# Optimization experiments

Hardware: AMD Instinct MI355X
Metric: run time of the kernel (lower is better)

## Reference

```python
import jax, jax.numpy as jnp
import numpy as np

N_NODES = 100000
N_EDGES = 1600000


def _glorot(key, shape):
    fan_in, fan_out = shape[0], shape[1]
    lim = np.sqrt(6.0 / (fan_in + fan_out))
    return jax.random.uniform(key, shape, jnp.float32, -lim, lim)


def setup_inputs() -> dict:
    key = jax.random.key(0)
    ks = jax.random.split(key, 8)
    x = jax.random.normal(ks[0], (N_NODES, 2), jnp.float32)
    edge_index = jax.random.randint(ks[1], (2, N_EDGES), 0, N_NODES, jnp.int32)
    return {
        "x": x,
        "edge_index": edge_index,
        "W1": _glorot(ks[2], (2, 64)),
        "b1": jnp.zeros((64,), jnp.float32),
        "W2": _glorot(ks[3], (64, 64)),
        "b2": jnp.zeros((64,), jnp.float32),
        "W3": _glorot(ks[4], (64, 64)),
        "b3": jnp.zeros((64,), jnp.float32),
        "fw1": _glorot(ks[5], (64, 128)),
        "fb1": jnp.zeros((128,), jnp.float32),
        "fw2": _glorot(ks[6], (128, 32)),
        "fb2": jnp.zeros((32,), jnp.float32),
    }


def _gcn_norm(edge_index, n_nodes, dtype):
    # PyG GCNConv default: add self-loops, symmetric normalization.
    loop = jnp.arange(n_nodes, dtype=edge_index.dtype)
    src = jnp.concatenate([edge_index[0], loop])
    dst = jnp.concatenate([edge_index[1], loop])
    deg = jax.ops.segment_sum(jnp.ones_like(dst, dtype), dst, num_segments=n_nodes)
    dinv = jnp.where(deg > 0, jax.lax.rsqrt(jnp.maximum(deg, 1e-12)), 0.0)
    norm = dinv[src] * dinv[dst]  # [E + N]
    return src, dst, norm


def _gcn_layer(h, src, dst, norm, n_nodes, W, b):
    h = h @ W                                   # [N, C_out] transform first (C_out small)
    msg = h[src] * norm[:, None]                # gather + per-edge scale
    out = jax.ops.segment_sum(msg, dst, num_segments=n_nodes)  # scatter-add
    return out + b


def reference(x, edge_index, W1, b1, W2, b2, W3, b3, fw1, fb1, fw2, fb2):
    n = x.shape[0]
    src, dst, norm = _gcn_norm(edge_index, n, x.dtype)
    h = jax.nn.relu(_gcn_layer(x, src, dst, norm, n, W1, b1))
    h = jax.nn.relu(_gcn_layer(h, src, dst, norm, n, W2, b2))
    h = jax.nn.relu(_gcn_layer(h, src, dst, norm, n, W3, b3))
    h = jax.nn.relu(h @ fw1 + fb1)  # fc1
    return h @ fw2 + fb2            # fc2 -> bottleneck latent
```

## Files before the change

kernel.cpp:

```cpp
#include <hip/hip_runtime.h>
#include <hip/hip_bf16.h>

#define NN 100000
#define NE 1600000
#define NBUK 1563
#define NBB  196
#define BATCH 8192
#define CNTSZ (NBUK*NBB)
#define SCANB 300

using bf16 = __hip_bfloat16;
typedef unsigned short us8_t __attribute__((ext_vector_type(8)));
static __device__ __forceinline__ float b2f(bf16 v){ return __bfloat162float(v); }
static __device__ __forceinline__ bf16 f2b(float v){ return __float2bfloat16(v); }
static __device__ __forceinline__ float us2f(unsigned u){
  unsigned x = u<<16; float f; __builtin_memcpy(&f,&x,4); return f;
}
static __device__ __forceinline__ unsigned short f2us(float v){
  bf16 b = f2b(v); unsigned short u; __builtin_memcpy(&u,&b,2); return u;
}

#define W1F   0
#define B1F   128
#define W2F   192
#define B2F   4288
#define W3F   4352
#define B3F   8448
#define FW1F  8512
#define FB1F  16704
#define FW2F  16832
#define FB2F  20928
#define WTOT  20960

__global__ void k_flag0(int* flag){ if(threadIdx.x==0) *flag = 0; }
__global__ void k_sniffB(const unsigned short* __restrict__ xr, int* flag){
  __shared__ int found;
  if(threadIdx.x==0) found = 0;
  __syncthreads();
  int loc = 0;
  for(int si = blockIdx.x*256 + threadIdx.x; si < 100000; si += 98*256){
    unsigned e = (xr[si*2]>>7)&0xFF;
    if(e==0xFFu || e==0u) loc = 1;
  }
  if(loc) found = 1;
  __syncthreads();
  if(threadIdx.x==0 && found) atomicOr(flag, 1);
}

__global__ void k_convert_w(const void* p0,const void* p1,const void* p2,const void* p3,
                            const void* p4,const void* p5,const void* p6,const void* p7,
                            const void* p8,const void* p9,
                            const int* __restrict__ flag, float* __restrict__ Wc){
  int t = blockIdx.x*256 + threadIdx.x;
  if(t >= WTOT) return;
  const void* ps[10] = {p0,p1,p2,p3,p4,p5,p6,p7,p8,p9};
  const int off[11] = {W1F,B1F,W2F,B2F,W3F,B3F,FW1F,FB1F,FW2F,FB2F,WTOT};
  int seg = 0;
  while(off[seg+1] <= t) seg++;
  int j = t - off[seg];
  Wc[t] = (*flag) ? ((const float*)ps[seg])[j] : b2f(((const bf16*)ps[seg])[j]);
}

__global__ void k_bhist(const int* __restrict__ dst, int* __restrict__ cnt){
  __shared__ int hist[NBUK];
  for(int j=threadIdx.x; j<NBUK; j+=512) hist[j] = 0;
  __syncthreads();
  int e0 = blockIdx.x*BATCH;
  int e1 = min(NE, e0+BATCH);
  int q0 = e0>>2, q1 = e1>>2;
  const int4* d4 = (const int4*)dst;
  for(int q=q0+threadIdx.x; q<q1; q+=512){
    int4 d = d4[q];
    atomicAdd(&hist[d.x>>6], 1);
    atomicAdd(&hist[d.y>>6], 1);
    atomicAdd(&hist[d.z>>6], 1);
    atomicAdd(&hist[d.w>>6], 1);
  }
  __syncthreads();
  for(int j=threadIdx.x; j<NBUK; j+=512) cnt[j*NBB + blockIdx.x] = hist[j];
}
__global__ void k_scanA(const int* __restrict__ cnt, int* __restrict__ tmp,
                        int* __restrict__ bsum){
  __shared__ int sh[1024];
  int gi = blockIdx.x*1024 + threadIdx.x;
  int v = (gi < CNTSZ) ? cnt[gi] : 0;
  sh[threadIdx.x] = v; __syncthreads();
  for(int off=1; off<1024; off<<=1){
    int t = (threadIdx.x>=off) ? sh[threadIdx.x-off] : 0;
    __syncthreads();
    sh[threadIdx.x] += t;
    __syncthreads();
  }
  if(gi < CNTSZ) tmp[gi] = sh[threadIdx.x];
  if(threadIdx.x == 1023) bsum[blockIdx.x] = sh[1023];
}
__global__ void k_scanB(const int* __restrict__ bsum, int* __restrict__ boff){
  __shared__ int sh[512];
  int v = (threadIdx.x < SCANB) ? bsum[threadIdx.x] : 0;
  sh[threadIdx.x] = v; __syncthreads();
  for(int off=1; off<512; off<<=1){
    int t = (threadIdx.x>=off) ? sh[threadIdx.x-off] : 0;
    __syncthreads();
    sh[threadIdx.x] += t;
    __syncthreads();
  }
  boff[threadIdx.x] = sh[threadIdx.x] - v;
}
__global__ void k_scanC(int* __restrict__ cnt, const int* __restrict__ tmp,
                        const int* __restrict__ boff, int* __restrict__ bucketStart){
  int gi = blockIdx.x*1024 + threadIdx.x;
  if(gi < CNTSZ){
    int orig = cnt[gi];
    int excl = tmp[gi] - orig + boff[gi>>10];
    cnt[gi] = excl;
    if(gi % NBB == 0) bucketStart[gi/NBB] = excl;
  }
  if(gi == 0) bucketStart[NBUK] = NE;
}
__global__ void k_bplace(const int* __restrict__ src, const int* __restrict__ dst,
                         const int* __restrict__ cnt, int* __restrict__ epk){
  __shared__ int cur[NBUK];
  for(int j=threadIdx.x; j<NBUK; j+=512) cur[j] = cnt[j*NBB + blockIdx.x];
  __syncthreads();
  int e0 = blockIdx.x*BATCH, e1 = min(NE, e0+BATCH);
  int q0 = e0>>2, q1 = e1>>2;
  const int4* d4 = (const int4*)dst;
  const int4* s4 = (const int4*)src;
  for(int q=q0+threadIdx.x; q<q1; q+=512){
    int4 d = d4[q];
    int4 s = s4[q];
    int p0 = atomicAdd(&cur[d.x>>6], 1);
    int p1 = atomicAdd(&cur[d.y>>6], 1);
    int p2 = atomicAdd(&cur[d.z>>6], 1);
    int p3 = atomicAdd(&cur[d.w>>6], 1);
    epk[p0] = (s.x<<6) | (d.x&63);
    epk[p1] = (s.y<<6) | (d.y&63);
    epk[p2] = (s.z<<6) | (d.z&63);
    epk[p3] = (s.w<<6) | (d.w&63);
  }
}
__global__ void k_bsort(const int* __restrict__ bucketStart, const int* __restrict__ epk,
                        int* __restrict__ srcS, int* __restrict__ rowptr,
                        float* __restrict__ dinv, const void* __restrict__ xv,
                        const int* __restrict__ flag, float2* __restrict__ xd){
  __shared__ int hist[64], excl[64], cur[64];
  int tid = threadIdx.x;
  if(tid < 64) hist[tid] = 0;
  __syncthreads();
  int b = blockIdx.x, beg = bucketStart[b], end = bucketStart[b+1];
  for(int p=beg+tid; p<end; p+=512) atomicAdd(&hist[epk[p]&63], 1);
  __syncthreads();
  if(tid == 0){
    int run = 0;
    for(int j=0;j<64;j++){ excl[j] = run; run += hist[j]; }
  }
  __syncthreads();
  if(tid < 64){
    int g = b*64 + tid;
    if(g < NN){
      rowptr[g] = beg + excl[tid];
      float d = rsqrtf((float)(hist[tid] + 1));
      dinv[g]  = d;
      float x0, x1;
      if(*flag){ float2 p = ((const float2*)xv)[g]; x0=p.x; x1=p.y; }
      else     { const bf16* xp=(const bf16*)xv; x0=b2f(xp[2*g]); x1=b2f(xp[2*g+1]); }
      xd[g] = make_float2(x0*d, x1*d);
    }
    cur[tid] = excl[tid];
  }
  if(b == 0 && tid == 0) rowptr[NN] = NE;
  __syncthreads();
  for(int p=beg+tid; p<end; p+=512){
    int pk = epk[p];
    int pos = atomicAdd(&cur[pk&63], 1);
    srcS[beg+pos] = pk>>6;
  }
}

__global__ void k_prop1(const int* __restrict__ rowptr, const int* __restrict__ srcS,
                        const float2* __restrict__ xd, const float* __restrict__ Wc,
                        const float* __restrict__ dinv, bf16* __restrict__ h){
  __shared__ float W1s[128];
  __shared__ float bs[64];
  if(threadIdx.x < 128) W1s[threadIdx.x] = Wc[W1F + threadIdx.x];
  if(threadIdx.x < 64)  bs[threadIdx.x]  = Wc[B1F + threadIdx.x];
  __syncthreads();
  int i = blockIdx.x*256 + threadIdx.x;
  if(i >= NN) return;
  int beg = rowptr[i], end = rowptr[i+1];
  float2 self = xd[i];
  float ax[8] = {self.x,0,0,0,0,0,0,0};
  float ay[8] = {self.y,0,0,0,0,0,0,0};
  int p = beg;
  for(; p+8 <= end; p += 8){
    int sI[8];
    #pragma unroll
    for(int j=0;j<8;j++) sI[j] = srcS[p+j];
    float2 v[8];
    #pragma unroll
    for(int j=0;j<8;j++) v[j] = xd[sI[j]];
    #pragma unroll
    for(int j=0;j<8;j++){ ax[j] += v[j].x; ay[j] += v[j].y; }
  }
  for(; p<end; p++){ float2 v=xd[srcS[p]]; ax[0]+=v.x; ay[0]+=v.y; }
  float y0 = ((ax[0]+ax[1])+(ax[2]+ax[3]))+((ax[4]+ax[5])+(ax[6]+ax[7]));
  float y1 = ((ay[0]+ay[1])+(ay[2]+ay[3]))+((ay[4]+ay[5])+(ay[6]+ay[7]));
  float d = dinv[i];
  unsigned short* hp = (unsigned short*)h + (size_t)i*64;
  #pragma unroll
  for(int g=0; g<8; g++){
    us8_t o;
    #pragma unroll
    for(int j=0;j<8;j++){
      int c = g*8+j;
      o[j] = f2us(fmaxf(d*(y0*W1s[c] + y1*W1s[64+c]) + bs[c], 0.0f));
    }
    *(us8_t*)(hp + g*8) = o;
  }
}

__global__ void __launch_bounds__(256) k_transform64(
    const bf16* __restrict__ h, const float* __restrict__ W,
    const float* __restrict__ dinv, bf16* __restrict__ s){
  __shared__ float Ws[64*64];
  __shared__ float hs[64][68];
  __shared__ float dl[64];
  int tid = threadIdx.x;
  for(int j=tid; j<4096; j+=256) Ws[j] = W[j];
  int row0 = blockIdx.x*64;
  if(tid < 64){ int r = row0+tid; dl[tid] = (r<NN)? dinv[r] : 0.0f; }
  for(int ch = tid; ch < 512; ch += 256){
    int r = ch>>3, c8 = (ch&7)*8;
    int gr = row0 + r;
    float f[8];
    if(gr < NN){
      us8_t v = *(const us8_t*)((const unsigned short*)h + (size_t)gr*64 + c8);
      #pragma unroll
      for(int j=0;j<8;j++) f[j] = us2f(v[j]);
    } else {
      #pragma unroll
      for(int j=0;j<8;j++) f[j] = 0.0f;
    }
    *(float4*)&hs[r][c8]   = make_float4(f[0],f[1],f[2],f[3]);
    *(float4*)&hs[r][c8+4] = make_float4(f[4],f[5],f[6],f[7]);
  }
  __syncthreads();
  int ty = tid>>4, tx = tid&15;
  float acc[4][4] = {{0}};
  #pragma unroll 8
  for(int k=0;k<64;k++){
    float4 b4 = *(const float4*)&Ws[k*64 + tx*4];
    float a0 = hs[ty*4+0][k];
    float a1 = hs[ty*4+1][k];
    float a2 = hs[ty*4+2][k];
    float a3 = hs[ty*4+3][k];
    acc[0][0] = fmaf(a0,b4.x,acc[0][0]); acc[0][1] = fmaf(a0,b4.y,acc[0][1]);
    acc[0][2] = fmaf(a0,b4.z,acc[0][2]); acc[0][3] = fmaf(a0,b4.w,acc[0][3]);
    acc[1][0] = fmaf(a1,b4.x,acc[1][0]); acc[1][1] = fmaf(a1,b4.y,acc[1][1]);
    acc[1][2] = fmaf(a1,b4.z,acc[1][2]); acc[1][3] = fmaf(a1,b4.w,acc[1][3]);
    acc[2][0] = fmaf(a2,b4.x,acc[2][0]); acc[2][1] = fmaf(a2,b4.y,acc[2][1]);
    acc[2][2] = fmaf(a2,b4.z,acc[2][2]); acc[2][3] = fmaf(a2,b4.w,acc[2][3]);
    acc[3][0] = fmaf(a3,b4.x,acc[3][0]); acc[3][1] = fmaf(a3,b4.y,acc[3][1]);
    acc[3][2] = fmaf(a3,b4.z,acc[3][2]); acc[3][3] = fmaf(a3,b4.w,acc[3][3]);
  }
  #pragma unroll
  for(int rr=0; rr<4; rr++){
    int r = row0 + ty*4 + rr;
    if(r < NN){
      float dv = dl[ty*4+rr];
      unsigned lo = f2us(acc[rr][0]*dv) | ((unsigned)f2us(acc[rr][1]*dv) << 16);
      unsigned hi = f2us(acc[rr][2]*dv) | ((unsigned)f2us(acc[rr][3]*dv) << 16);
      uint2 o; o.x = lo; o.y = hi;
      *(uint2*)((unsigned short*)s + (size_t)r*64 + tx*4) = o;
    }
  }
}

__global__ void __launch_bounds__(256) k_aggregate(
    const int* __restrict__ rowptr, const int* __restrict__ srcS,
    const bf16* __restrict__ s, const float* __restrict__ dinv,
    const float* __restrict__ bias, bf16* __restrict__ h){
  int wave = threadIdx.x>>6, lane = threadIdx.x&63;
  int half = lane>>5;
  int lh   = lane&31;
  int slot = lh>>3;
  int oct  = lane&7;
  int i = blockIdx.x*8 + wave*2 + half;
  int beg = rowptr[i], end = rowptr[i+1];
  unsigned deg = (unsigned)(end - beg);
  const unsigned short* sp = (const unsigned short*)s;
  us8_t sv = *(const us8_t*)(sp + (size_t)i*64 + oct*8);
  float a0[8] = {0,0,0,0,0,0,0,0};
  float a1[8] = {0,0,0,0,0,0,0,0};
  int p0 = beg & ~3;
  while(__any(p0 < end)){
    if(p0 < end){
      int q  = p0 + slot*4;
      int qc = min(q, NE-4);
      int4 E = *(const int4*)(srcS + qc);
      us8_t v0 = *(const us8_t*)(sp + (size_t)E.x*64 + oct*8);
      us8_t v1 = *(const us8_t*)(sp + (size_t)E.y*64 + oct*8);
      us8_t v2 = *(const us8_t*)(sp + (size_t)E.z*64 + oct*8);
      us8_t v3 = *(const us8_t*)(sp + (size_t)E.w*64 + oct*8);
      unsigned rel = (unsigned)(q - beg);
      if(rel+0u < deg){
        #pragma unroll
        for(int j=0;j<8;j++) a0[j] += us2f(v0[j]);
      }
      if(rel+1u < deg){
        #pragma unroll
        for(int j=0;j<8;j++) a1[j] += us2f(v1[j]);
      }
      if(rel+2u < deg){
        #pragma unroll
        for(int j=0;j<8;j++) a0[j] += us2f(v2[j]);
      }
      if(rel+3u < deg){
        #pragma unroll
        for(int j=0;j<8;j++) a1[j] += us2f(v3[j]);
      }
    }
    p0 += 16;
  }
  float c[8];
  #pragma unroll
  for(int j=0;j<8;j++){
    float v = a0[j] + a1[j];
    v += __shfl_xor(v, 8, 64);
    v += __shfl_xor(v, 16, 64);
    c[j] = v;
  }
  float dv = dinv[i];
  float4 bA = *(const float4*)(bias + oct*8);
  float4 bB = *(const float4*)(bias + oct*8 + 4);
  float bb[8] = {bA.x,bA.y,bA.z,bA.w,bB.x,bB.y,bB.z,bB.w};
  us8_t o;
  #pragma unroll
  for(int j=0;j<8;j++){
    float v = c[j] + us2f(sv[j]);
    o[j] = f2us(fmaxf(fmaf(dv, v, bb[j]), 0.0f));
  }
  if(slot == 0)
    *(us8_t*)((unsigned short*)h + (size_t)i*64 + oct*8) = o;
}

__global__ void __launch_bounds__(256) k_fc1(const bf16* __restrict__ h,
                                             const float* __restrict__ Wc,
                                             bf16* __restrict__ f){
  __shared__ float W1s[64*128];
  __shared__ float hs[64][68];
  __shared__ float bs[128];
  int tid = threadIdx.x;
  for(int j=tid; j<8192; j+=256) W1s[j] = Wc[FW1F+j];
  if(tid < 128) bs[tid] = Wc[FB1F+tid];
  int row0 = blockIdx.x*64;
  for(int ch = tid; ch < 512; ch += 256){
    int r = ch>>3, c8 = (ch&7)*8, gr = row0 + r;
    float fv[8];
    if(gr < NN){
      us8_t v = *(const us8_t*)((const unsigned short*)h + (size_t)gr*64 + c8);
      #pragma unroll
      for(int j=0;j<8;j++) fv[j] = us2f(v[j]);
    } else {
      #pragma unroll
      for(int j=0;j<8;j++) fv[j] = 0.0f;
    }
    *(float4*)&hs[r][c8]   = make_float4(fv[0],fv[1],fv[2],fv[3]);
    *(float4*)&hs[r][c8+4] = make_float4(fv[4],fv[5],fv[6],fv[7]);
  }
  __syncthreads();
  int ty = tid>>4, tx = tid&15;
  float acc[4][8] = {{0}};
  #pragma unroll 4
  for(int k=0;k<64;k++){
    float4 b0 = *(const float4*)&W1s[k*128 + tx*8];
    float4 b1 = *(const float4*)&W1s[k*128 + tx*8 + 4];
    float a0 = hs[ty*4+0][k], a1 = hs[ty*4+1][k];
    float a2 = hs[ty*4+2][k], a3 = hs[ty*4+3][k];
    acc[0][0]=fmaf(a0,b0.x,acc[0][0]); acc[0][1]=fmaf(a0,b0.y,acc[0][1]);
    acc[0][2]=fmaf(a0,b0.z,acc[0][2]); acc[0][3]=fmaf(a0,b0.w,acc[0][3]);
    acc[0][4]=fmaf(a0,b1.x,acc[0][4]); acc[0][5]=fmaf(a0,b1.y,acc[0][5]);
    acc[0][6]=fmaf(a0,b1.z,acc[0][6]); acc[0][7]=fmaf(a0,b1.w,acc[0][7]);
    acc[1][0]=fmaf(a1,b0.x,acc[1][0]); acc[1][1]=fmaf(a1,b0.y,acc[1][1]);
    acc[1][2]=fmaf(a1,b0.z,acc[1][2]); acc[1][3]=fmaf(a1,b0.w,acc[1][3]);
    acc[1][4]=fmaf(a1,b1.x,acc[1][4]); acc[1][5]=fmaf(a1,b1.y,acc[1][5]);
    acc[1][6]=fmaf(a1,b1.z,acc[1][6]); acc[1][7]=fmaf(a1,b1.w,acc[1][7]);
    acc[2][0]=fmaf(a2,b0.x,acc[2][0]); acc[2][1]=fmaf(a2,b0.y,acc[2][1]);
    acc[2][2]=fmaf(a2,b0.z,acc[2][2]); acc[2][3]=fmaf(a2,b0.w,acc[2][3]);
    acc[2][4]=fmaf(a2,b1.x,acc[2][4]); acc[2][5]=fmaf(a2,b1.y,acc[2][5]);
    acc[2][6]=fmaf(a2,b1.z,acc[2][6]); acc[2][7]=fmaf(a2,b1.w,acc[2][7]);
    acc[3][0]=fmaf(a3,b0.x,acc[3][0]); acc[3][1]=fmaf(a3,b0.y,acc[3][1]);
    acc[3][2]=fmaf(a3,b0.z,acc[3][2]); acc[3][3]=fmaf(a3,b0.w,acc[3][3]);
    acc[3][4]=fmaf(a3,b1.x,acc[3][4]); acc[3][5]=fmaf(a3,b1.y,acc[3][5]);
    acc[3][6]=fmaf(a3,b1.z,acc[3][6]); acc[3][7]=fmaf(a3,b1.w,acc[3][7]);
  }
  #pragma unroll
  for(int r=0;r<4;r++){
    int gr = row0 + ty*4 + r;
    if(gr < NN){
      us8_t o;
      #pragma unroll
      for(int j=0;j<8;j++) o[j] = f2us(fmaxf(acc[r][j] + bs[tx*8+j], 0.0f));
      *(us8_t*)((unsigned short*)f + (size_t)gr*128 + tx*8) = o;
    }
  }
}

__global__ void __launch_bounds__(256) k_fc2(const bf16* __restrict__ f,
                                             const float* __restrict__ Wc,
                                             const int* __restrict__ flag,
                                             void* __restrict__ outv){
  __shared__ float W2s[128*32];
  __shared__ float fs[64][132];
  __shared__ float bs[32];
  int tid = threadIdx.x;
  for(int j=tid; j<4096; j+=256) W2s[j] = Wc[FW2F+j];
  if(tid < 32) bs[tid] = Wc[FB2F+tid];
  int row0 = blockIdx.x*64;
  for(int ch = tid; ch < 1024; ch += 256){
    int r = ch>>4, c8 = (ch&15)*8, gr = row0 + r;
    float fv[8];
    if(gr < NN){
      us8_t v = *(const us8_t*)((const unsigned short*)f + (size_t)gr*128 + c8);
      #pragma unroll
      for(int j=0;j<8;j++) fv[j] = us2f(v[j]);
    } else {
      #pragma unroll
      for(int j=0;j<8;j++) fv[j] = 0.0f;
    }
    *(float4*)&fs[r][c8]   = make_float4(fv[0],fv[1],fv[2],fv[3]);
    *(float4*)&fs[r][c8+4] = make_float4(fv[4],fv[5],fv[6],fv[7]);
  }
  __syncthreads();
  int ty = tid>>3, tx = tid&7;
  float acc[2][4] = {{0}};
  #pragma unroll 8
  for(int k=0;k<128;k++){
    float4 b4 = *(const float4*)&W2s[k*32 + tx*4];
    float a0 = fs[ty*2+0][k], a1 = fs[ty*2+1][k];
    acc[0][0]=fmaf(a0,b4.x,acc[0][0]); acc[0][1]=fmaf(a0,b4.y,acc[0][1]);
    acc[0][2]=fmaf(a0,b4.z,acc[0][2]); acc[0][3]=fmaf(a0,b4.w,acc[0][3]);
    acc[1][0]=fmaf(a1,b4.x,acc[1][0]); acc[1][1]=fmaf(a1,b4.y,acc[1][1]);
    acc[1][2]=fmaf(a1,b4.z,acc[1][2]); acc[1][3]=fmaf(a1,b4.w,acc[1][3]);
  }
  int fl = *flag;
  #pragma unroll
  for(int r=0;r<2;r++){
    int gr = row0 + ty*2 + r;
    if(gr < NN){
      float o0 = acc[r][0]+bs[tx*4+0], o1 = acc[r][1]+bs[tx*4+1];
      float o2 = acc[r][2]+bs[tx*4+2], o3 = acc[r][3]+bs[tx*4+3];
      if(fl){
        *(float4*)((float*)outv + (size_t)gr*32 + tx*4) = make_float4(o0,o1,o2,o3);
      } else {
        unsigned lo = f2us(o0) | ((unsigned)f2us(o1)<<16);
        unsigned hi = f2us(o2) | ((unsigned)f2us(o3)<<16);
        uint2 o; o.x = lo; o.y = hi;
        *(uint2*)((unsigned short*)outv + (size_t)gr*32 + tx*4) = o;
      }
    }
  }
}

extern "C" void kernel_launch(void* const* d_in, const int* in_sizes, int n_in,
                              void* d_out, int out_size, void* d_ws, size_t ws_size,
                              hipStream_t stream){
  const void* x   = d_in[0];
  const int*  ei  = (const int*)d_in[1];
  const int* srcI = ei;
  const int* dstI = ei + NE;

  char*   base   = (char*)d_ws;
  int*    flag   = (int*)   (base + 0);
  float*  Wc     = (float*) (base + 256);
  int*    bstart = (int*)   (base + 84224);
  int*    cnt    = (int*)   (base + 90624);
  int*    tmpS   = (int*)   (base + 1316096);
  int*    bsum   = (int*)   (base + 2541568);
  int*    boff   = (int*)   (base + 2543616);
  float*  dinv   = (float*) (base + 2545664);
  int*    rowptr = (int*)   (base + 2945664);
  int*    epk    = (int*)   (base + 3345792);
  int*    srcS   = (int*)   (base + 9745792);
  float2* xd     = (float2*)(base + 16145792);
  bf16*   s      = (bf16*)  (base + 16945792);
  bf16*   h      = (bf16*)  (base + 29745792);
  bf16*   f      = (bf16*)  (base + 42545792);

  k_flag0    <<<1, 64, 0, stream>>>(flag);
  k_sniffB   <<<98, 256, 0, stream>>>((const unsigned short*)x, flag);
  k_convert_w<<<(WTOT+255)/256, 256, 0, stream>>>(
      d_in[2], d_in[3], d_in[4], d_in[5], d_in[6],
      d_in[7], d_in[8], d_in[9], d_in[10], d_in[11], flag, Wc);

  k_bhist <<<NBB, 512, 0, stream>>>(dstI, cnt);
  k_scanA <<<SCANB, 1024, 0, stream>>>(cnt, tmpS, bsum);
  k_scanB <<<1, 512, 0, stream>>>(bsum, boff);
  k_scanC <<<SCANB, 1024, 0, stream>>>(cnt, tmpS, boff, bstart);
  k_bplace<<<NBB, 512, 0, stream>>>(srcI, dstI, cnt, epk);
  k_bsort <<<NBUK, 512, 0, stream>>>(bstart, epk, srcS, rowptr, dinv, x, flag, xd);

  k_prop1<<<(NN+255)/256, 256, 0, stream>>>(rowptr, srcS, xd, Wc, dinv, h);

  k_transform64<<<(NN+63)/64, 256, 0, stream>>>(h, Wc+W2F, dinv, s);
  k_aggregate  <<<NN/8, 256, 0, stream>>>(rowptr, srcS, s, dinv, Wc+B2F, h);

  k_transform64<<<(NN+63)/64, 256, 0, stream>>>(h, Wc+W3F, dinv, s);
  k_aggregate  <<<NN/8, 256, 0, stream>>>(rowptr, srcS, s, dinv, Wc+B3F, h);

  k_fc1<<<(NN+63)/64, 256, 0, stream>>>(h, Wc, f);
  k_fc2<<<(NN+63)/64, 256, 0, stream>>>(f, Wc, flag, d_out);
}
```

Baseline: 311.3 us.

## Replace per-block bucket histograms with global atomics and a single-block scan

The bucketing step for the edge sort no longer builds per-block shared histograms with a multi-kernel scan over 1563x196 counts. It now counts edges per bucket with global atomics, scans the 1563 totals in one block, and places edges using global atomic cursors. The flag-reset and sniff kernels are merged into one single-block kernel that also zeroes the counts, and the dinv and bias loads in the aggregate kernel are hoisted ahead of the edge loop. This removes several launches and about 2.4 MB of count traffic, but adds heavy global atomic contention on about 1.5k counters. Edge order inside a bucket also becomes nondeterministic, which can change floating-point summation order.

```diff
diff --git a/kernel.cpp b/kernel.cpp
--- a/kernel.cpp
+++ b/kernel.cpp
@@ -6,8 +6,6 @@
 #define NBUK 1563
 #define NBB  196
 #define BATCH 8192
-#define CNTSZ (NBUK*NBB)
-#define SCANB 300
 
 using bf16 = __hip_bfloat16;
 typedef unsigned short us8_t __attribute__((ext_vector_type(8)));
@@ -32,19 +30,21 @@
 #define FB2F  20928
 #define WTOT  20960
 
-__global__ void k_flag0(int* flag){ if(threadIdx.x==0) *flag = 0; }
-__global__ void k_sniffB(const unsigned short* __restrict__ xr, int* flag){
+__global__ void k_fsniff(const unsigned short* __restrict__ xr, int* __restrict__ flag,
+                         int* __restrict__ cnt){
   __shared__ int found;
-  if(threadIdx.x==0) found = 0;
+  int t = threadIdx.x;
+  if(t==0) found = 0;
+  for(int j=t; j<NBUK; j+=1024) cnt[j] = 0;
   __syncthreads();
   int loc = 0;
-  for(int si = blockIdx.x*256 + threadIdx.x; si < 100000; si += 98*256){
+  for(int si=t; si<NN; si+=1024){
     unsigned e = (xr[si*2]>>7)&0xFF;
     if(e==0xFFu || e==0u) loc = 1;
   }
   if(loc) found = 1;
   __syncthreads();
-  if(threadIdx.x==0 && found) atomicOr(flag, 1);
+  if(t==0) *flag = found;
 }
 
 __global__ void k_convert_w(const void* p0,const void* p1,const void* p2,const void* p3,
@@ -61,67 +61,42 @@
   Wc[t] = (*flag) ? ((const float*)ps[seg])[j] : b2f(((const bf16*)ps[seg])[j]);
 }
 
-__global__ void k_bhist(const int* __restrict__ dst, int* __restrict__ cnt){
-  __shared__ int hist[NBUK];
-  for(int j=threadIdx.x; j<NBUK; j+=512) hist[j] = 0;
-  __syncthreads();
+__global__ void k_count(const int* __restrict__ dst, int* __restrict__ cnt){
   int e0 = blockIdx.x*BATCH;
   int e1 = min(NE, e0+BATCH);
   int q0 = e0>>2, q1 = e1>>2;
   const int4* d4 = (const int4*)dst;
   for(int q=q0+threadIdx.x; q<q1; q+=512){
     int4 d = d4[q];
-    atomicAdd(&hist[d.x>>6], 1);
-    atomicAdd(&hist[d.y>>6], 1);
-    atomicAdd(&hist[d.z>>6], 1);
-    atomicAdd(&hist[d.w>>6], 1);
-  }
-  __syncthreads();
-  for(int j=threadIdx.x; j<NBUK; j+=512) cnt[j*NBB + blockIdx.x] = hist[j];
-}
-__global__ void k_scanA(const int* __restrict__ cnt, int* __restrict__ tmp,
-                        int* __restrict__ bsum){
-  __shared__ int sh[1024];
-  int gi = blockIdx.x*1024 + threadIdx.x;
-  int v = (gi < CNTSZ) ? cnt[gi] : 0;
-  sh[threadIdx.x] = v; __syncthreads();
-  for(int off=1; off<1024; off<<=1){
-    int t = (threadIdx.x>=off) ? sh[threadIdx.x-off] : 0;
+    atomicAdd(&cnt[d.x>>6], 1);
+    atomicAdd(&cnt[d.y>>6], 1);
+    atomicAdd(&cnt[d.z>>6], 1);
+    atomicAdd(&cnt[d.w>>6], 1);
+  }
+}
+__global__ void k_scan1(int* __restrict__ cnt, int* __restrict__ bucketStart){
+  __shared__ int A[2048], B[2048];
+  int t = threadIdx.x;
+  int v0 = (t      < NBUK) ? cnt[t]      : 0;
+  int v1 = (t+1024 < NBUK) ? cnt[t+1024] : 0;
+  A[t] = v0; A[t+1024] = v1;
+  __syncthreads();
+  int* src = A; int* dstb = B;
+  for(int off=1; off<2048; off<<=1){
+    int i0 = t, i1 = t+1024;
+    dstb[i0] = src[i0] + ((i0>=off)? src[i0-off] : 0);
+    dstb[i1] = src[i1] + ((i1>=off)? src[i1-off] : 0);
     __syncthreads();
-    sh[threadIdx.x] += t;
-    __syncthreads();
-  }
-  if(gi < CNTSZ) tmp[gi] = sh[threadIdx.x];
-  if(threadIdx.x == 1023) bsum[blockIdx.x] = sh[1023];
-}
-__global__ void k_scanB(const int* __restrict__ bsum, int* __restrict__ boff){
-  __shared__ int sh[512];
-  int v = (threadIdx.x < SCANB) ? bsum[threadIdx.x] : 0;
-  sh[threadIdx.x] = v; __syncthreads();
-  for(int off=1; off<512; off<<=1){
-    int t = (threadIdx.x>=off) ? sh[threadIdx.x-off] : 0;
-    __syncthreads();
-    sh[threadIdx.x] += t;
-    __syncthreads();
-  }
-  boff[threadIdx.x] = sh[threadIdx.x] - v;
-}
-__global__ void k_scanC(int* __restrict__ cnt, const int* __restrict__ tmp,
-                        const int* __restrict__ boff, int* __restrict__ bucketStart){
-  int gi = blockIdx.x*1024 + threadIdx.x;
-  if(gi < CNTSZ){
-    int orig = cnt[gi];
-    int excl = tmp[gi] - orig + boff[gi>>10];
-    cnt[gi] = excl;
-    if(gi % NBB == 0) bucketStart[gi/NBB] = excl;
-  }
-  if(gi == 0) bucketStart[NBUK] = NE;
-}
-__global__ void k_bplace(const int* __restrict__ src, const int* __restrict__ dst,
-                         const int* __restrict__ cnt, int* __restrict__ epk){
-  __shared__ int cur[NBUK];
-  for(int j=threadIdx.x; j<NBUK; j+=512) cur[j] = cnt[j*NBB + blockIdx.x];
-  __syncthreads();
+    int* tmp = src; src = dstb; dstb = tmp;
+  }
+  int e0 = src[t] - v0;
+  int e1 = src[t+1024] - v1;
+  if(t < NBUK){ cnt[t] = e0; bucketStart[t] = e0; }
+  if(t+1024 < NBUK){ cnt[t+1024] = e1; bucketStart[t+1024] = e1; }
+  if(t+1024 == NBUK) bucketStart[NBUK] = e1;
+}
+__global__ void k_place(const int* __restrict__ src, const int* __restrict__ dst,
+                        int* __restrict__ cnt, int* __restrict__ epk){
   int e0 = blockIdx.x*BATCH, e1 = min(NE, e0+BATCH);
   int q0 = e0>>2, q1 = e1>>2;
   const int4* d4 = (const int4*)dst;
@@ -129,10 +104,10 @@
   for(int q=q0+threadIdx.x; q<q1; q+=512){
     int4 d = d4[q];
     int4 s = s4[q];
-    int p0 = atomicAdd(&cur[d.x>>6], 1);
-    int p1 = atomicAdd(&cur[d.y>>6], 1);
-    int p2 = atomicAdd(&cur[d.z>>6], 1);
-    int p3 = atomicAdd(&cur[d.w>>6], 1);
+    int p0 = atomicAdd(&cnt[d.x>>6], 1);
+    int p1 = atomicAdd(&cnt[d.y>>6], 1);
+    int p2 = atomicAdd(&cnt[d.z>>6], 1);
+    int p3 = atomicAdd(&cnt[d.w>>6], 1);
     epk[p0] = (s.x<<6) | (d.x&63);
     epk[p1] = (s.y<<6) | (d.y&63);
     epk[p2] = (s.z<<6) | (d.z&63);
@@ -290,6 +265,9 @@
   unsigned deg = (unsigned)(end - beg);
   const unsigned short* sp = (const unsigned short*)s;
   us8_t sv = *(const us8_t*)(sp + (size_t)i*64 + oct*8);
+  float dv = dinv[i];
+  float4 bA = *(const float4*)(bias + oct*8);
+  float4 bB = *(const float4*)(bias + oct*8 + 4);
   float a0[8] = {0,0,0,0,0,0,0,0};
   float a1[8] = {0,0,0,0,0,0,0,0};
   int p0 = beg & ~3;
@@ -330,9 +308,6 @@
     v += __shfl_xor(v, 16, 64);
     c[j] = v;
   }
-  float dv = dinv[i];
-  float4 bA = *(const float4*)(bias + oct*8);
-  float4 bB = *(const float4*)(bias + oct*8 + 4);
   float bb[8] = {bA.x,bA.y,bA.z,bA.w,bB.x,bB.y,bB.z,bB.w};
   us8_t o;
   #pragma unroll
@@ -475,9 +450,6 @@
   float*  Wc     = (float*) (base + 256);
   int*    bstart = (int*)   (base + 84224);
   int*    cnt    = (int*)   (base + 90624);
-  int*    tmpS   = (int*)   (base + 1316096);
-  int*    bsum   = (int*)   (base + 2541568);
-  int*    boff   = (int*)   (base + 2543616);
   float*  dinv   = (float*) (base + 2545664);
   int*    rowptr = (int*)   (base + 2945664);
   int*    epk    = (int*)   (base + 3345792);
@@ -487,18 +459,15 @@
   bf16*   h      = (bf16*)  (base + 29745792);
   bf16*   f      = (bf16*)  (base + 42545792);
 
-  k_flag0    <<<1, 64, 0, stream>>>(flag);
-  k_sniffB   <<<98, 256, 0, stream>>>((const unsigned short*)x, flag);
+  k_fsniff   <<<1, 1024, 0, stream>>>((const unsigned short*)x, flag, cnt);
   k_convert_w<<<(WTOT+255)/256, 256, 0, stream>>>(
       d_in[2], d_in[3], d_in[4], d_in[5], d_in[6],
       d_in[7], d_in[8], d_in[9], d_in[10], d_in[11], flag, Wc);
 
-  k_bhist <<<NBB, 512, 0, stream>>>(dstI, cnt);
-  k_scanA <<<SCANB, 1024, 0, stream>>>(cnt, tmpS, bsum);
-  k_scanB <<<1, 512, 0, stream>>>(bsum, boff);
-  k_scanC <<<SCANB, 1024, 0, stream>>>(cnt, tmpS, boff, bstart);
-  k_bplace<<<NBB, 512, 0, stream>>>(srcI, dstI, cnt, epk);
-  k_bsort <<<NBUK, 512, 0, stream>>>(bstart, epk, srcS, rowptr, dinv, x, flag, xd);
+  k_count<<<NBB, 512, 0, stream>>>(dstI, cnt);
+  k_scan1<<<1, 1024, 0, stream>>>(cnt, bstart);
+  k_place<<<NBB, 512, 0, stream>>>(srcI, dstI, cnt, epk);
+  k_bsort<<<NBUK, 512, 0, stream>>>(bstart, epk, srcS, rowptr, dinv, x, flag, xd);
 
   k_prop1<<<(NN+255)/256, 256, 0, stream>>>(rowptr, srcS, xd, Wc, dinv, h);
 
```

Measured after the change: 791.2 us. 2.54x slower.

## Use bf16 MFMA with hi/lo split weights for dense transforms and FC layers

Applied to the files above, without the earlier changes.

Replaces the shared-memory FP32 FMA tiled GEMMs in the two 64x64 transforms, fc1 and fc2 with MFMA 16x16x32 bf16 instructions. Weights are pre-transposed into bf16 high and low halves so accuracy stays near fp32, with activations already in bf16. This removes the shared-memory staging and syncs, at the cost of an extra conversion kernel and narrower, strided 2-byte output stores.

```diff
diff --git a/kernel.cpp b/kernel.cpp
--- a/kernel.cpp
+++ b/kernel.cpp
@@ -11,6 +11,8 @@
 
 using bf16 = __hip_bfloat16;
 typedef unsigned short us8_t __attribute__((ext_vector_type(8)));
+typedef short s8v __attribute__((ext_vector_type(8)));
+typedef float f4v __attribute__((ext_vector_type(4)));
 static __device__ __forceinline__ float b2f(bf16 v){ return __bfloat162float(v); }
 static __device__ __forceinline__ bf16 f2b(float v){ return __float2bfloat16(v); }
 static __device__ __forceinline__ float us2f(unsigned u){
@@ -31,6 +33,16 @@
 #define FW2F  16832
 #define FB2F  20928
 #define WTOT  20960
+
+#define W2TH  0
+#define W2TL  4096
+#define W3TH  8192
+#define W3TL  12288
+#define F1TH  16384
+#define F1TL  24576
+#define F2TH  32768
+#define F2TL  36864
+#define WBTOT 40960
 
 __global__ void k_flag0(int* flag){ if(threadIdx.x==0) *flag = 0; }
 __global__ void k_sniffB(const unsigned short* __restrict__ xr, int* flag){
@@ -59,6 +71,28 @@
   while(off[seg+1] <= t) seg++;
   int j = t - off[seg];
   Wc[t] = (*flag) ? ((const float*)ps[seg])[j] : b2f(((const bf16*)ps[seg])[j]);
+}
+
+__global__ void k_convert_t(const float* __restrict__ Wc, unsigned short* __restrict__ Wb){
+  int t = blockIdx.x*256 + threadIdx.x;
+  if(t >= 20480) return;
+  float v; int dhi, dlo;
+  if(t < 4096){
+    int c = t>>6, k = t&63;
+    v = Wc[W2F + k*64 + c];  dhi = W2TH + t; dlo = W2TL + t;
+  } else if(t < 8192){
+    int t2 = t-4096; int c = t2>>6, k = t2&63;
+    v = Wc[W3F + k*64 + c];  dhi = W3TH + t2; dlo = W3TL + t2;
+  } else if(t < 16384){
+    int t2 = t-8192; int c = t2>>6, k = t2&63;
+    v = Wc[FW1F + k*128 + c]; dhi = F1TH + t2; dlo = F1TL + t2;
+  } else {
+    int t2 = t-16384; int c = t2>>7, k = t2&127;
+    v = Wc[FW2F + k*32 + c]; dhi = F2TH + t2; dlo = F2TL + t2;
+  }
+  unsigned short hi = f2us(v);
+  Wb[dhi] = hi;
+  Wb[dlo] = f2us(v - us2f(hi));
 }
 
 __global__ void k_bhist(const int* __restrict__ dst, int* __restrict__ cnt){
@@ -220,58 +254,41 @@
 }
 
 __global__ void __launch_bounds__(256) k_transform64(
-    const bf16* __restrict__ h, const float* __restrict__ W,
+    const bf16* __restrict__ h, const unsigned short* __restrict__ wth,
+    const unsigned short* __restrict__ wtl,
     const float* __restrict__ dinv, bf16* __restrict__ s){
-  __shared__ float Ws[64*64];
-  __shared__ float hs[64][68];
-  __shared__ float dl[64];
   int tid = threadIdx.x;
-  for(int j=tid; j<4096; j+=256) Ws[j] = W[j];
-  int row0 = blockIdx.x*64;
-  if(tid < 64){ int r = row0+tid; dl[tid] = (r<NN)? dinv[r] : 0.0f; }
-  for(int ch = tid; ch < 512; ch += 256){
-    int r = ch>>3, c8 = (ch&7)*8;
-    int gr = row0 + r;
-    float f[8];
-    if(gr < NN){
-      us8_t v = *(const us8_t*)((const unsigned short*)h + (size_t)gr*64 + c8);
-      #pragma unroll
-      for(int j=0;j<8;j++) f[j] = us2f(v[j]);
-    } else {
-      #pragma unroll
-      for(int j=0;j<8;j++) f[j] = 0.0f;
-    }
-    *(float4*)&hs[r][c8]   = make_float4(f[0],f[1],f[2],f[3]);
-    *(float4*)&hs[r][c8+4] = make_float4(f[4],f[5],f[6],f[7]);
-  }
-  __syncthreads();
-  int ty = tid>>4, tx = tid&15;
-  float acc[4][4] = {{0}};
-  #pragma unroll 8
-  for(int k=0;k<64;k++){
-    float4 b4 = *(const float4*)&Ws[k*64 + tx*4];
-    float a0 = hs[ty*4+0][k];
-    float a1 = hs[ty*4+1][k];
-    float a2 = hs[ty*4+2][k];
-    float a3 = hs[ty*4+3][k];
-    acc[0][0] = fmaf(a0,b4.x,acc[0][0]); acc[0][1] = fmaf(a0,b4.y,acc[0][1]);
-    acc[0][2] = fmaf(a0,b4.z,acc[0][2]); acc[0][3] = fmaf(a0,b4.w,acc[0][3]);
-    acc[1][0] = fmaf(a1,b4.x,acc[1][0]); acc[1][1] = fmaf(a1,b4.y,acc[1][1]);
-    acc[1][2] = fmaf(a1,b4.z,acc[1][2]); acc[1][3] = fmaf(a1,b4.w,acc[1][3]);
-    acc[2][0] = fmaf(a2,b4.x,acc[2][0]); acc[2][1] = fmaf(a2,b4.y,acc[2][1]);
-    acc[2][2] = fmaf(a2,b4.z,acc[2][2]); acc[2][3] = fmaf(a2,b4.w,acc[2][3]);
-    acc[3][0] = fmaf(a3,b4.x,acc[3][0]); acc[3][1] = fmaf(a3,b4.y,acc[3][1]);
-    acc[3][2] = fmaf(a3,b4.z,acc[3][2]); acc[3][3] = fmaf(a3,b4.w,acc[3][3]);
-  }
-  #pragma unroll
-  for(int rr=0; rr<4; rr++){
-    int r = row0 + ty*4 + rr;
-    if(r < NN){
-      float dv = dl[ty*4+rr];
-      unsigned lo = f2us(acc[rr][0]*dv) | ((unsigned)f2us(acc[rr][1]*dv) << 16);
-      unsigned hi = f2us(acc[rr][2]*dv) | ((unsigned)f2us(acc[rr][3]*dv) << 16);
-      uint2 o; o.x = lo; o.y = hi;
-      *(uint2*)((unsigned short*)s + (size_t)r*64 + tx*4) = o;
+  int w = tid>>6, l = tid&63;
+  int lr = l&15, lg = l>>4;
+  int row0 = blockIdx.x*64 + w*16;
+  const unsigned short* hp = (const unsigned short*)h;
+  int arow = min(row0 + lr, NN-1);
+  s8v a0 = *(const s8v*)(hp + (size_t)arow*64 + lg*8);
+  s8v a1 = *(const s8v*)(hp + (size_t)arow*64 + 32 + lg*8);
+  f4v z = {0.f,0.f,0.f,0.f};
+  f4v acc0=z, acc1=z, acc2=z, acc3=z;
+  #define T64_TILE(ACC, C) { \
+    int wb = ((C)*16+lr)*64 + lg*8; \
+    s8v bh0 = *(const s8v*)(wth + wb); \
+    s8v bh1 = *(const s8v*)(wth + wb + 32); \
+    s8v bl0 = *(const s8v*)(wtl + wb); \
+    s8v bl1 = *(const s8v*)(wtl + wb + 32); \
+    ACC = __builtin_amdgcn_mfma_f32_16x16x32_bf16(a0, bh0, ACC, 0,0,0); \
+    ACC = __builtin_amdgcn_mfma_f32_16x16x32_bf16(a1, bh1, ACC, 0,0,0); \
+    ACC = __builtin_amdgcn_mfma_f32_16x16x32_bf16(a0, bl0, ACC, 0,0,0); \
+    ACC = __builtin_amdgcn_mfma_f32_16x16x32_bf16(a1, bl1, ACC, 0,0,0); }
+  T64_TILE(acc0, 0) T64_TILE(acc1, 1) T64_TILE(acc2, 2) T64_TILE(acc3, 3)
+  #undef T64_TILE
+  #pragma unroll
+  for(int r=0;r<4;r++){
+    int orow = row0 + lg*4 + r;
+    if(orow < NN){
+      float dv = dinv[orow];
+      unsigned short* op = (unsigned short*)s + (size_t)orow*64 + lr;
+      op[0]  = f2us(acc0[r]*dv);
+      op[16] = f2us(acc1[r]*dv);
+      op[32] = f2us(acc2[r]*dv);
+      op[48] = f2us(acc3[r]*dv);
     }
   }
 }
@@ -345,118 +362,98 @@
 }
 
 __global__ void __launch_bounds__(256) k_fc1(const bf16* __restrict__ h,
+                                             const unsigned short* __restrict__ wth,
+                                             const unsigned short* __restrict__ wtl,
                                              const float* __restrict__ Wc,
                                              bf16* __restrict__ f){
-  __shared__ float W1s[64*128];
-  __shared__ float hs[64][68];
-  __shared__ float bs[128];
   int tid = threadIdx.x;
-  for(int j=tid; j<8192; j+=256) W1s[j] = Wc[FW1F+j];
-  if(tid < 128) bs[tid] = Wc[FB1F+tid];
-  int row0 = blockIdx.x*64;
-  for(int ch = tid; ch < 512; ch += 256){
-    int r = ch>>3, c8 = (ch&7)*8, gr = row0 + r;
-    float fv[8];
-    if(gr < NN){
-      us8_t v = *(const us8_t*)((const unsigned short*)h + (size_t)gr*64 + c8);
+  int w = tid>>6, l = tid&63;
+  int lr = l&15, lg = l>>4;
+  int row0 = blockIdx.x*64 + w*16;
+  const unsigned short* hp = (const unsigned short*)h;
+  int arow = min(row0 + lr, NN-1);
+  s8v a0 = *(const s8v*)(hp + (size_t)arow*64 + lg*8);
+  s8v a1 = *(const s8v*)(hp + (size_t)arow*64 + 32 + lg*8);
+  f4v z = {0.f,0.f,0.f,0.f};
+  f4v acc[8] = {z,z,z,z,z,z,z,z};
+  float bias[8];
+  #pragma unroll
+  for(int c=0;c<8;c++){
+    int wb = (c*16+lr)*64 + lg*8;
+    s8v bh0 = *(const s8v*)(wth + wb);
+    s8v bh1 = *(const s8v*)(wth + wb + 32);
+    s8v bl0 = *(const s8v*)(wtl + wb);
+    s8v bl1 = *(const s8v*)(wtl + wb + 32);
+    acc[c] = __builtin_amdgcn_mfma_f32_16x16x32_bf16(a0, bh0, acc[c], 0,0,0);
+    acc[c] = __builtin_amdgcn_mfma_f32_16x16x32_bf16(a1, bh1, acc[c], 0,0,0);
+    acc[c] = __builtin_amdgcn_mfma_f32_16x16x32_bf16(a0, bl0, acc[c], 0,0,0);
+    acc[c] = __builtin_amdgcn_mfma_f32_16x16x32_bf16(a1, bl1, acc[c], 0,0,0);
+    bias[c] = Wc[FB1F + c*16 + lr];
+  }
+  #pragma unroll
+  for(int r=0;r<4;r++){
+    int orow = row0 + lg*4 + r;
+    if(orow < NN){
+      unsigned short* op = (unsigned short*)f + (size_t)orow*128 + lr;
       #pragma unroll
-      for(int j=0;j<8;j++) fv[j] = us2f(v[j]);
-    } else {
-      #pragma unroll
-      for(int j=0;j<8;j++) fv[j] = 0.0f;
+      for(int c=0;c<8;c++) op[c*16] = f2us(fmaxf(acc[c][r] + bias[c], 0.0f));
     }
-    *(float4*)&hs[r][c8]   = make_float4(fv[0],fv[1],fv[2],fv[3]);
-    *(float4*)&hs[r][c8+4] = make_float4(fv[4],fv[5],fv[6],fv[7]);
-  }
-  __syncthreads();
-  int ty = tid>>4, tx = tid&15;
-  float acc[4][8] = {{0}};
-  #pragma unroll 4
-  for(int k=0;k<64;k++){
-    float4 b0 = *(const float4*)&W1s[k*128 + tx*8];
-    float4 b1 = *(const float4*)&W1s[k*128 + tx*8 + 4];
-    float a0 = hs[ty*4+0][k], a1 = hs[ty*4+1][k];
-    float a2 = hs[ty*4+2][k], a3 = hs[ty*4+3][k];
-    acc[0][0]=fmaf(a0,b0.x,acc[0][0]); acc[0][1]=fmaf(a0,b0.y,acc[0][1]);
-    acc[0][2]=fmaf(a0,b0.z,acc[0][2]); acc[0][3]=fmaf(a0,b0.w,acc[0][3]);
-    acc[0][4]=fmaf(a0,b1.x,acc[0][4]); acc[0][5]=fmaf(a0,b1.y,acc[0][5]);
-    acc[0][6]=fmaf(a0,b1.z,acc[0][6]); acc[0][7]=fmaf(a0,b1.w,acc[0][7]);
-    acc[1][0]=fmaf(a1,b0.x,acc[1][0]); acc[1][1]=fmaf(a1,b0.y,acc[1][1]);
-    acc[1][2]=fmaf(a1,b0.z,acc[1][2]); acc[1][3]=fmaf(a1,b0.w,acc[1][3]);
-    acc[1][4]=fmaf(a1,b1.x,acc[1][4]); acc[1][5]=fmaf(a1,b1.y,acc[1][5]);
-    acc[1][6]=fmaf(a1,b1.z,acc[1][6]); acc[1][7]=fmaf(a1,b1.w,acc[1][7]);
-    acc[2][0]=fmaf(a2,b0.x,acc[2][0]); acc[2][1]=fmaf(a2,b0.y,acc[2][1]);
-    acc[2][2]=fmaf(a2,b0.z,acc[2][2]); acc[2][3]=fmaf(a2,b0.w,acc[2][3]);
-    acc[2][4]=fmaf(a2,b1.x,acc[2][4]); acc[2][5]=fmaf(a2,b1.y,acc[2][5]);
-    acc[2][6]=fmaf(a2,b1.z,acc[2][6]); acc[2][7]=fmaf(a2,b1.w,acc[2][7]);
-    acc[3][0]=fmaf(a3,b0.x,acc[3][0]); acc[3][1]=fmaf(a3,b0.y,acc[3][1]);
-    acc[3][2]=fmaf(a3,b0.z,acc[3][2]); acc[3][3]=fmaf(a3,b0.w,acc[3][3]);
-    acc[3][4]=fmaf(a3,b1.x,acc[3][4]); acc[3][5]=fmaf(a3,b1.y,acc[3][5]);
-    acc[3][6]=fmaf(a3,b1.z,acc[3][6]); acc[3][7]=fmaf(a3,b1.w,acc[3][7]);
-  }
-  #pragma unroll
-  for(int r=0;r<4;r++){
-    int gr = row0 + ty*4 + r;
-    if(gr < NN){
-      us8_t o;
-      #pragma unroll
-      for(int j=0;j<8;j++) o[j] = f2us(fmaxf(acc[r][j] + bs[tx*8+j], 0.0f));
-      *(us8_t*)((unsigned short*)f + (size_t)gr*128 + tx*8) = o;
-    }
   }
 }
 
 __global__ void __launch_bounds__(256) k_fc2(const bf16* __restrict__ f,
+                                             const unsigned short* __restrict__ wth,
+                                             const unsigned short* __restrict__ wtl,
                                              const float* __restrict__ Wc,
                                              const int* __restrict__ flag,
                                              void* __restrict__ outv){
-  __shared__ float W2s[128*32];
-  __shared__ float fs[64][132];
-  __shared__ float bs[32];
   int tid = threadIdx.x;
-  for(int j=tid; j<4096; j+=256) W2s[j] = Wc[FW2F+j];
-  if(tid < 32) bs[tid] = Wc[FB2F+tid];
-  int row0 = blockIdx.x*64;
-  for(int ch = tid; ch < 1024; ch += 256){
-    int r = ch>>4, c8 = (ch&15)*8, gr = row0 + r;
-    float fv[8];
-    if(gr < NN){
-      us8_t v = *(const us8_t*)((const unsigned short*)f + (size_t)gr*128 + c8);
-      #pragma unroll
-      for(int j=0;j<8;j++) fv[j] = us2f(v[j]);
-    } else {
-      #pragma unroll
-      for(int j=0;j<8;j++) fv[j] = 0.0f;
-    }
-    *(float4*)&fs[r][c8]   = make_float4(fv[0],fv[1],fv[2],fv[3]);
-    *(float4*)&fs[r][c8+4] = make_float4(fv[4],fv[5],fv[6],fv[7]);
-  }
-  __syncthreads();
-  int ty = tid>>3, tx = tid&7;
-  float acc[2][4] = {{0}};
-  #pragma unroll 8
-  for(int k=0;k<128;k++){
-    float4 b4 = *(const float4*)&W2s[k*32 + tx*4];
-    float a0 = fs[ty*2+0][k], a1 = fs[ty*2+1][k];
-    acc[0][0]=fmaf(a0,b4.x,acc[0][0]); acc[0][1]=fmaf(a0,b4.y,acc[0][1]);
-    acc[0][2]=fmaf(a0,b4.z,acc[0][2]); acc[0][3]=fmaf(a0,b4.w,acc[0][3]);
-    acc[1][0]=fmaf(a1,b4.x,acc[1][0]); acc[1][1]=fmaf(a1,b4.y,acc[1][1]);
-    acc[1][2]=fmaf(a1,b4.z,acc[1][2]); acc[1][3]=fmaf(a1,b4.w,acc[1][3]);
+  int w = tid>>6, l = tid&63;
+  int lr = l&15, lg = l>>4;
+  int row0 = blockIdx.x*64 + w*16;
+  const unsigned short* fp = (const unsigned short*)f;
+  int arow = min(row0 + lr, NN-1);
+  s8v a0 = *(const s8v*)(fp + (size_t)arow*128 + lg*8);
+  s8v a1 = *(const s8v*)(fp + (size_t)arow*128 + 32 + lg*8);
+  s8v a2 = *(const s8v*)(fp + (size_t)arow*128 + 64 + lg*8);
+  s8v a3 = *(const s8v*)(fp + (size_t)arow*128 + 96 + lg*8);
+  f4v z = {0.f,0.f,0.f,0.f};
+  f4v acc[2] = {z,z};
+  float bias[2];
+  #pragma unroll
+  for(int c=0;c<2;c++){
+    int wb = (c*16+lr)*128 + lg*8;
+    s8v bh0 = *(const s8v*)(wth + wb);
+    s8v bh1 = *(const s8v*)(wth + wb + 32);
+    s8v bh2 = *(const s8v*)(wth + wb + 64);
+    s8v bh3 = *(const s8v*)(wth + wb + 96);
+    s8v bl0 = *(const s8v*)(wtl + wb);
+    s8v bl1 = *(const s8v*)(wtl + wb + 32);
+    s8v bl2 = *(const s8v*)(wtl + wb + 64);
+    s8v bl3 = *(const s8v*)(wtl + wb + 96);
+    acc[c] = __builtin_amdgcn_mfma_f32_16x16x32_bf16(a0, bh0, acc[c], 0,0,0);
+    acc[c] = __builtin_amdgcn_mfma_f32_16x16x32_bf16(a1, bh1, acc[c], 0,0,0);
+    acc[c] = __builtin_amdgcn_mfma_f32_16x16x32_bf16(a2, bh2, acc[c], 0,0,0);
+    acc[c] = __builtin_amdgcn_mfma_f32_16x16x32_bf16(a3, bh3, acc[c], 0,0,0);
+    acc[c] = __builtin_amdgcn_mfma_f32_16x16x32_bf16(a0, bl0, acc[c], 0,0,0);
+    acc[c] = __builtin_amdgcn_mfma_f32_16x16x32_bf16(a1, bl1, acc[c], 0,0,0);
+    acc[c] = __builtin_amdgcn_mfma_f32_16x16x32_bf16(a2, bl2, acc[c], 0,0,0);
+    acc[c] = __builtin_amdgcn_mfma_f32_16x16x32_bf16(a3, bl3, acc[c], 0,0,0);
+    bias[c] = Wc[FB2F + c*16 + lr];
   }
   int fl = *flag;
   #pragma unroll
-  for(int r=0;r<2;r++){
-    int gr = row0 + ty*2 + r;
-    if(gr < NN){
-      float o0 = acc[r][0]+bs[tx*4+0], o1 = acc[r][1]+bs[tx*4+1];
-      float o2 = acc[r][2]+bs[tx*4+2], o3 = acc[r][3]+bs[tx*4+3];
+  for(int r=0;r<4;r++){
+    int orow = row0 + lg*4 + r;
+    if(orow < NN){
       if(fl){
-        *(float4*)((float*)outv + (size_t)gr*32 + tx*4) = make_float4(o0,o1,o2,o3);
+        float* op = (float*)outv + (size_t)orow*32 + lr;
+        op[0]  = acc[0][r] + bias[0];
+        op[16] = acc[1][r] + bias[1];
       } else {
-        unsigned lo = f2us(o0) | ((unsigned)f2us(o1)<<16);
-        unsigned hi = f2us(o2) | ((unsigned)f2us(o3)<<16);
-        uint2 o; o.x = lo; o.y = hi;
-        *(uint2*)((unsigned short*)outv + (size_t)gr*32 + tx*4) = o;
+        unsigned short* op = (unsigned short*)outv + (size_t)orow*32 + lr;
+        op[0]  = f2us(acc[0][r] + bias[0]);
+        op[16] = f2us(acc[1][r] + bias[1]);
       }
     }
   }
@@ -486,12 +483,14 @@
   bf16*   s      = (bf16*)  (base + 16945792);
   bf16*   h      = (bf16*)  (base + 29745792);
   bf16*   f      = (bf16*)  (base + 42545792);
+  unsigned short* Wb = (unsigned short*)(base + 68145792);
 
   k_flag0    <<<1, 64, 0, stream>>>(flag);
   k_sniffB   <<<98, 256, 0, stream>>>((const unsigned short*)x, flag);
   k_convert_w<<<(WTOT+255)/256, 256, 0, stream>>>(
       d_in[2], d_in[3], d_in[4], d_in[5], d_in[6],
       d_in[7], d_in[8], d_in[9], d_in[10], d_in[11], flag, Wc);
+  k_convert_t<<<80, 256, 0, stream>>>(Wc, Wb);
 
   k_bhist <<<NBB, 512, 0, stream>>>(dstI, cnt);
   k_scanA <<<SCANB, 1024, 0, stream>>>(cnt, tmpS, bsum);
@@ -502,12 +501,12 @@
 
   k_prop1<<<(NN+255)/256, 256, 0, stream>>>(rowptr, srcS, xd, Wc, dinv, h);
 
-  k_transform64<<<(NN+63)/64, 256, 0, stream>>>(h, Wc+W2F, dinv, s);
+  k_transform64<<<NBUK, 256, 0, stream>>>(h, Wb+W2TH, Wb+W2TL, dinv, s);
   k_aggregate  <<<NN/8, 256, 0, stream>>>(rowptr, srcS, s, dinv, Wc+B2F, h);
 
-  k_transform64<<<(NN+63)/64, 256, 0, stream>>>(h, Wc+W3F, dinv, s);
+  k_transform64<<<NBUK, 256, 0, stream>>>(h, Wb+W3TH, Wb+W3TL, dinv, s);
   k_aggregate  <<<NN/8, 256, 0, stream>>>(rowptr, srcS, s, dinv, Wc+B3F, h);
 
-  k_fc1<<<(NN+63)/64, 256, 0, stream>>>(h, Wc, f);
-  k_fc2<<<(NN+63)/64, 256, 0, stream>>>(f, Wc, flag, d_out);
-}
+  k_fc1<<<NBUK, 256, 0, stream>>>(h, Wb+F1TH, Wb+F1TL, Wc, f);
+  k_fc2<<<NBUK, 256, 0, stream>>>(f, Wb+F2TH, Wb+F2TL, Wc, flag, d_out);
+}
```

Result: no change. 316.5 us (+1.7%).
